# Optimization experiments

Hardware: AMD Instinct MI355X
Metric: run time of the kernel (lower is better)

## Reference

```python
import jax, jax.numpy as jnp
import numpy as np

TEMPERATURE = 0.1
GAMMA = 0.5
LOSS_WEIGHT = 1.0
MAX_BATCH_SIZE = 5000
POS_DIST_THRESH = 1.0
NEG_SAMPLE_RATIO = 2.0
EPS_NORM = 1e-8   # torch cosine_similarity norm clamp
EPS_POS = 1e-6


def setup_inputs() -> dict:
    key = jax.random.key(0)
    k1, k2 = jax.random.split(key)
    N, D = 15000, 64
    features = jax.random.normal(k1, (N, D), dtype=jnp.float32)
    # xyz coords in a 20-unit box -> ~8 positive neighbors per point at thresh 1.0
    coords = jax.random.uniform(k2, (N, 3), dtype=jnp.float32) * 20.0
    # all points are power-line class (label 2) so M = N statically
    labels = jnp.full((N,), 2, dtype=jnp.int32)
    return {"features": features, "labels": labels, "coords": coords}


def reference(features, labels, coords):
    # labels are all == 2 and none == ignore_index, so the boolean selections
    # (ignore_index filter, line_mask) are identities: line_feats = features.
    M = features.shape[0]
    # row-normalized features for cosine similarity (torch eps=1e-8 clamp)
    fnorm = features / jnp.maximum(
        jnp.linalg.norm(features, axis=1, keepdims=True), EPS_NORM)
    sq = jnp.sum(coords * coords, axis=1)  # [M]

    total_nce = jnp.float32(0.0)
    total_cont = jnp.float32(0.0)
    col = jnp.arange(M)[None, :]
    for start in range(0, M, MAX_BATCH_SIZE):
        end = min(start + MAX_BATCH_SIZE, M)
        B = end - start
        # [B, M] pairwise cosine similarity
        feat_sim = fnorm[start:end] @ fnorm.T
        # [B, M] euclidean cdist via ||a||^2 + ||b||^2 - 2 a.b
        d2 = sq[start:end, None] + sq[None, :] - 2.0 * (coords[start:end] @ coords.T)
        coord_dist = jnp.sqrt(jnp.maximum(d2, 0.0))
        pos = (coord_dist < POS_DIST_THRESH) & (coord_dist > 1e-6)
        posf = pos.astype(feat_sim.dtype)
        negf = 1.0 - posf

        exp_sim = jnp.exp(feat_sim / TEMPERATURE)
        # k = min(int(neg_sample_ratio * max positives per row), M); traced scalar
        max_neg = (NEG_SAMPLE_RATIO * pos.sum(axis=1).max()).astype(jnp.int32)
        k = jnp.minimum(max_neg, M)
        # top-k sum of masked negatives: full descending sort + length-k row mask
        vals = jnp.sort(exp_sim * negf, axis=1)[:, ::-1]
        sum_exp = jnp.sum(jnp.where(col < k, vals, 0.0), axis=1)

        pos_sum = jnp.sum(exp_sim * posf, axis=1)
        batch_nce = jnp.mean(-jnp.log(pos_sum / (sum_exp + pos_sum + EPS_POS)))
        batch_cont = jnp.mean(jnp.abs((1.0 - feat_sim) - coord_dist) * posf)

        total_nce = total_nce + batch_nce * B
        total_cont = total_cont + batch_cont * B

    loss = (total_nce / M + GAMMA * (total_cont / M)) * LOSS_WEIGHT
    return loss
```

## Files before the change

### kernel.cpp

```cpp
#include <hip/hip_runtime.h>
#include <math.h>

#define NPTS 15000
#define NPAD 15360
#define DIM 64
#define BATCH 5000
#define QT 64
#define NCH 4
#define NBLKQ 235
#define NGB (NBLKQ * NCH)
#define NPB 1875
#define BLKM 512
#define NT (NPAD / 16)
#define NTC (NT / NCH)
#define CAPE 12
#define NCELL 8000
#define NBIN 320
#define HW 160
#define GHW ((size_t)NBLKQ * QT * HW)
#define T_G 0.26f
#define KEY_BASE 0x3E80u

typedef __attribute__((ext_vector_type(8))) short bf16x8;
typedef __attribute__((ext_vector_type(4))) float f32x4;

__device__ __forceinline__ float bf2f(unsigned u) {
  return __uint_as_float(u << 16);
}

__global__ __launch_bounds__(256) void k_norm(const float* __restrict__ feat,
                                              const float* __restrict__ coords,
                                              unsigned short* __restrict__ fbf,
                                              float4* __restrict__ c4,
                                              uint4* __restrict__ ghist4,
                                              int* __restrict__ batch_max,
                                              float* __restrict__ out) {
  unsigned gz = blockIdx.x * 256 + threadIdx.x;
  if (gz < (unsigned)(GHW / 4)) ghist4[gz] = make_uint4(0, 0, 0, 0);
  if (gz == 0) { out[0] = 0.0f; batch_max[0] = 0; batch_max[1] = 0; batch_max[2] = 0; }
  int i = blockIdx.x * 4 + (threadIdx.x >> 6);
  int d = threadIdx.x & 63;
  float v = (i < NPTS) ? feat[i * DIM + d] : 0.0f;
  float ss = v * v;
#pragma unroll
  for (int off = 32; off; off >>= 1) ss += __shfl_down(ss, off);
  ss = __shfl(ss, 0);
  float m = fmaxf(sqrtf(ss), 1e-8f);
  float nv = v / m;
  unsigned u = __float_as_uint(nv);
  fbf[i * DIM + d] = (unsigned short)((u + 0x7FFFu + ((u >> 16) & 1u)) >> 16);
  if (d == 0) {
    float cx = (i < NPTS) ? coords[i * 3] : 0.0f;
    float cy = (i < NPTS) ? coords[i * 3 + 1] : 0.0f;
    float cz = (i < NPTS) ? coords[i * 3 + 2] : 0.0f;
    c4[i] = make_float4(cx, cy, cz, cx * cx + cy * cy + cz * cz);
  }
}

__device__ __forceinline__ int cell_of(float4 c) {
  int cx = min(19, max(0, (int)c.x));
  int cy = min(19, max(0, (int)c.y));
  int cz = min(19, max(0, (int)c.z));
  return cx + 20 * (cy + 20 * cz);
}

__global__ __launch_bounds__(1024) void k_cells(const float4* __restrict__ c4,
                                                int* __restrict__ cell_start,
                                                int* __restrict__ cell_cnt,
                                                int* __restrict__ pts) {
  __shared__ int s_cnt[NCELL];
  __shared__ int s_ptr[NCELL];
  __shared__ int sw[16];
  int tid = threadIdx.x, lane = tid & 63, wv = tid >> 6;
  for (int x = tid; x < NCELL; x += 1024) s_cnt[x] = 0;
  __syncthreads();
  for (int i = tid; i < NPTS; i += 1024) atomicAdd(&s_cnt[cell_of(c4[i])], 1);
  __syncthreads();
  int run = 0;
  for (int c = 0; c < NCELL; c += 1024) {
    int idx = c + tid;
    int v = (idx < NCELL) ? s_cnt[idx] : 0;
    int inc = v;
#pragma unroll
    for (int off = 1; off < 64; off <<= 1) {
      int o = __shfl_up(inc, off);
      if (lane >= off) inc += o;
    }
    if (lane == 63) sw[wv] = inc;
    __syncthreads();
    int woff = 0, tot = 0;
#pragma unroll
    for (int w = 0; w < 16; ++w) {
      int s = sw[w];
      if (w < wv) woff += s;
      tot += s;
    }
    __syncthreads();
    int excl = run + woff + inc - v;
    if (idx < NCELL) {
      cell_start[idx] = excl;
      cell_cnt[idx] = v;
      s_ptr[idx] = excl;
    }
    run += tot;
  }
  __syncthreads();
  for (int i = tid; i < NPTS; i += 1024) {
    int ix = atomicAdd(&s_ptr[cell_of(c4[i])], 1);
    pts[ix] = i;
  }
}

union SMem {
  unsigned hist[QT * HW];
  struct { int ec[8]; unsigned short ek[8][CAPE]; int pc[8]; } p;
};

__global__ __launch_bounds__(BLKM, 4) void k_main(const unsigned short* __restrict__ fbf,
                                                  const float4* __restrict__ c4,
                                                  const int* __restrict__ cell_start,
                                                  const int* __restrict__ cell_cnt,
                                                  const int* __restrict__ pts,
                                                  unsigned* __restrict__ ghist,
                                                  float* __restrict__ g_ps,
                                                  float* __restrict__ row_cont,
                                                  int* __restrict__ batch_max,
                                                  unsigned short* __restrict__ excl_keys,
                                                  int* __restrict__ excl_cnt) {
  __shared__ SMem sm;
  int bx = blockIdx.x;
  int tid = threadIdx.x;
  int wv = tid >> 6, lane = tid & 63;

  if (bx < NGB) {
    int tile = bx >> 2, ch = bx & 3;
    int i0 = tile * QT;
    int l15 = lane & 15, quad = lane >> 4;

    for (int x = tid; x < QT * HW; x += BLKM) sm.hist[x] = 0;

    bf16x8 aL[4], aH[4];
#pragma unroll
    for (int m = 0; m < 4; ++m) {
      const unsigned short* qrow = fbf + (size_t)(i0 + m * 16 + l15) * DIM + quad * 8;
      aL[m] = *(const bf16x8*)qrow;
      aH[m] = *(const bf16x8*)(qrow + 32);
    }
    __syncthreads();

    int tEnd = (ch + 1) * NTC;
    int t = ch * NTC + wv;
    const unsigned short* jr = fbf + (size_t)(t * 16 + l15) * DIM + quad * 8;
    bf16x8 bLo = *(const bf16x8*)jr;
    bf16x8 bHi = *(const bf16x8*)(jr + 32);
    for (; t < tEnd; t += 8) {
      int tn = (t + 8 < tEnd) ? t + 8 : t;
      const unsigned short* nr = fbf + (size_t)(tn * 16 + l15) * DIM + quad * 8;
      bf16x8 nLo = *(const bf16x8*)nr;
      bf16x8 nHi = *(const bf16x8*)(nr + 32);
      f32x4 acc[4];
#pragma unroll
      for (int m = 0; m < 4; ++m) {
        f32x4 a = {0.f, 0.f, 0.f, 0.f};
        a = __builtin_amdgcn_mfma_f32_16x16x32_bf16(aL[m], bLo, a, 0, 0, 0);
        a = __builtin_amdgcn_mfma_f32_16x16x32_bf16(aH[m], bHi, a, 0, 0, 0);
        acc[m] = a;
      }
#pragma unroll
      for (int m = 0; m < 4; ++m) {
#pragma unroll
        for (int r = 0; r < 4; ++r) {
          float s = acc[m][r];
          if (s >= T_G) {
            int q = m * 16 + quad * 4 + r;
            unsigned bin = (__float_as_uint(s) >> 16) - KEY_BASE;
            atomicAdd(&sm.hist[q * HW + (bin >> 1)], 1u << ((bin & 1) << 4));
          }
        }
      }
      bLo = nLo;
      bHi = nHi;
    }
    __syncthreads();

    unsigned* gh = ghist + (size_t)i0 * HW;
    for (int x = tid; x < QT * HW; x += BLKM) {
      unsigned v = sm.hist[x];
      if (v) atomicAdd(&gh[x], v);
    }
  } else {
    int bp = bx - NGB;
    int i = bp * 8 + wv;
    if (lane == 0) sm.p.ec[wv] = 0;
    float4 ci = c4[i];
    int cx = min(19, max(0, (int)ci.x));
    int cy = min(19, max(0, (int)ci.y));
    int cz = min(19, max(0, (int)ci.z));
    float psum = 0.f, csum = 0.f;
    int pc = 0;
    if (lane < 27) {
      int gx = cx + lane % 3 - 1, gy = cy + (lane / 3) % 3 - 1, gz = cz + lane / 9 - 1;
      if (gx >= 0 && gx < 20 && gy >= 0 && gy < 20 && gz >= 0 && gz < 20) {
        int cell = gx + 20 * (gy + 20 * gz);
        int s0 = cell_start[cell], e0 = s0 + cell_cnt[cell];
        for (int p = s0; p < e0; ++p) {
          int j = pts[p];
          if (j == i) continue;
          float4 cj = c4[j];
          float ddx = ci.x - cj.x, ddy = ci.y - cj.y, ddz = ci.z - cj.z;
          float d2 = ddx * ddx + ddy * ddy + ddz * ddz;
          if (d2 < 1.0f) {
            const unsigned short* fi = fbf + (size_t)i * DIM;
            const unsigned short* fj = fbf + (size_t)j * DIM;
            float dot = 0.f;
#pragma unroll
            for (int chv = 0; chv < 8; ++chv) {
              bf16x8 a = *(const bf16x8*)(fi + chv * 8);
              bf16x8 b = *(const bf16x8*)(fj + chv * 8);
#pragma unroll
              for (int e = 0; e < 8; ++e)
                dot = fmaf(bf2f((unsigned short)a[e] & 0xFFFFu),
                           bf2f((unsigned short)b[e] & 0xFFFFu), dot);
            }
            pc++;
            psum += expf(dot * 10.0f);
            csum += fabsf((1.0f - dot) - sqrtf(d2));
            if (dot >= T_G) {
              int ix = atomicAdd(&sm.p.ec[wv], 1);
              if (ix < CAPE) sm.p.ek[wv][ix] = (unsigned short)(__float_as_uint(dot) >> 16);
            }
          }
        }
      }
    }
#pragma unroll
    for (int off = 32; off; off >>= 1) {
      psum += __shfl_down(psum, off);
      csum += __shfl_down(csum, off);
      pc += __shfl_down(pc, off);
    }
    if (lane == 0) sm.p.pc[wv] = pc;
    __syncthreads();
    int ec = min(sm.p.ec[wv], CAPE);
    if (lane == 0) {
      g_ps[i] = psum;
      row_cont[i] = csum;
      excl_cnt[i] = ec;
    }
    for (int x = lane; x < ec; x += 64) excl_keys[(size_t)i * CAPE + x] = sm.p.ek[wv][x];
    if (tid == 0) {
      int m = 0;
#pragma unroll
      for (int w = 0; w < 8; ++w) m = max(m, sm.p.pc[w]);
      atomicMax(&batch_max[(bp * 8) / BATCH], m);
    }
  }
}

__global__ __launch_bounds__(BLKM) void k_select(const unsigned* __restrict__ ghist,
                                                 const float* __restrict__ g_ps,
                                                 const float* __restrict__ row_cont,
                                                 const int* __restrict__ batch_max,
                                                 const unsigned short* __restrict__ excl_keys,
                                                 const int* __restrict__ excl_cnt,
                                                 float* __restrict__ out) {
  int i0 = blockIdx.x * QT;
  int tid = threadIdx.x;
  int wv = tid >> 6, lane = tid & 63;
  float a_acc = 0.f, b_acc = 0.f;

  for (int qq = 0; qq < 8; ++qq) {
    int iq = i0 + wv * 8 + qq;
    if (iq >= NPTS) continue;
    int kq = min((int)(2.0f * (float)batch_max[iq / BATCH]), NPTS);
    int e = 5 * lane;
    const unsigned* hw_ = ghist + (size_t)iq * HW + (e >> 1);
    unsigned w0 = hw_[0], w1 = hw_[1], w2 = hw_[2];
    bool odd = (lane & 1) != 0;
    int h0 = (int)(odd ? (w0 >> 16) : (w0 & 0xFFFFu));
    int h1 = (int)(odd ? (w1 & 0xFFFFu) : (w0 >> 16));
    int h2 = (int)(odd ? (w1 >> 16) : (w1 & 0xFFFFu));
    int h3 = (int)(odd ? (w2 & 0xFFFFu) : (w1 >> 16));
    int h4 = (int)(odd ? (w2 >> 16) : (w2 & 0xFFFFu));
    int ec = min(excl_cnt[iq], CAPE);
    for (int ee = 0; ee < ec; ++ee) {
      unsigned key = excl_keys[(size_t)iq * CAPE + ee];
      unsigned bin = key - KEY_BASE;
      if (bin > NBIN - 1u) bin = NBIN - 1u;
      int c = (int)bin - e;
      if (c == 0) h0 = max(h0 - 1, 0);
      else if (c == 1) h1 = max(h1 - 1, 0);
      else if (c == 2) h2 = max(h2 - 1, 0);
      else if (c == 3) h3 = max(h3 - 1, 0);
      else if (c == 4) h4 = max(h4 - 1, 0);
    }
    int lsum = h0 + h1 + h2 + h3 + h4;
    int pre = lsum;
#pragma unroll
    for (int off = 1; off < 64; off <<= 1) {
      int o = __shfl_up(pre, off);
      if (lane >= off) pre += o;
    }
    int total = __shfl(pre, 63);
    int tke = min(kq, total);
    int cum = total - pre;
    float se = 0.0f;
    unsigned kb = KEY_BASE + (unsigned)e;
    {
      int tk4 = min(max(tke - cum, 0), h4); cum += h4;
      int tk3 = min(max(tke - cum, 0), h3); cum += h3;
      int tk2 = min(max(tke - cum, 0), h2); cum += h2;
      int tk1 = min(max(tke - cum, 0), h1); cum += h1;
      int tk0 = min(max(tke - cum, 0), h0);
      if (tk4) se += (float)tk4 * expf(10.0f * bf2f(kb + 4));
      if (tk3) se += (float)tk3 * expf(10.0f * bf2f(kb + 3));
      if (tk2) se += (float)tk2 * expf(10.0f * bf2f(kb + 2));
      if (tk1) se += (float)tk1 * expf(10.0f * bf2f(kb + 1));
      if (tk0) se += (float)tk0 * expf(10.0f * bf2f(kb + 0));
    }
#pragma unroll
    for (int off = 32; off; off >>= 1) se += __shfl_down(se, off);
    if (lane == 0) {
      float ps = g_ps[iq];
      float nce = -logf(ps / (se + ps + 1e-6f));
      if (!(nce < 1e30f)) nce = 0.0f;
      a_acc += nce;
      b_acc += row_cont[iq];
    }
  }
  __shared__ float sa[8], sb[8];
  if (lane == 0) { sa[wv] = a_acc; sb[wv] = b_acc; }
  __syncthreads();
  if (tid == 0) {
    float a = 0.f, b = 0.f;
#pragma unroll
    for (int w = 0; w < 8; ++w) { a += sa[w]; b += sb[w]; }
    atomicAdd(out, a / 15000.0f + 0.5f * ((b / 15000.0f) / 15000.0f));
  }
}

extern "C" void kernel_launch(void* const* d_in, const int* in_sizes, int n_in,
                              void* d_out, int out_size, void* d_ws, size_t ws_size,
                              hipStream_t stream) {
  const float* feat   = (const float*)d_in[0];
  const float* coords = (const float*)d_in[2];
  float* out = (float*)d_out;

  char* ws              = (char*)d_ws;
  unsigned short* fbf   = (unsigned short*)ws;
  float4* c4            = (float4*)(fbf + NPAD * DIM);
  float* row_cont       = (float*)(c4 + NPAD);
  float* g_ps           = row_cont + NPTS;
  int*   excl_ct        = (int*)(g_ps + NPTS);
  unsigned short* exclk = (unsigned short*)(excl_ct + NPTS);
  int*   batch_max      = (int*)(exclk + (size_t)NPTS * CAPE);
  unsigned* ghist       = (unsigned*)(batch_max + 4);
  int*   cell_start     = (int*)(ghist + GHW);
  int*   cell_cnt       = cell_start + NCELL;
  int*   pts            = cell_cnt + NCELL;

  k_norm<<<dim3(NPAD / 4), dim3(256), 0, stream>>>(feat, coords, fbf, c4,
                                                   (uint4*)ghist, batch_max, out);
  k_cells<<<dim3(1), dim3(1024), 0, stream>>>(c4, cell_start, cell_cnt, pts);
  k_main<<<dim3(NGB + NPB), dim3(BLKM), 0, stream>>>(fbf, c4, cell_start, cell_cnt, pts,
                                                     ghist, g_ps, row_cont, batch_max,
                                                     exclk, excl_ct);
  k_select<<<dim3(NBLKQ), dim3(BLKM), 0, stream>>>(ghist, g_ps, row_cont, batch_max,
                                                   exclk, excl_ct, out);
}
```

Baseline: 209.6 us.

## Compact positive pairs into shared list and compute dots one-per-lane in fp32

The positive-pair path now gathers neighbor indices and squared distances into a per-wave shared list, then lets each lane compute one pair's dot product. Before, at most 27 lanes each walked a cell serially, computing dots as they went. Dots now use the original fp32 features scaled by a precomputed inverse norm instead of bf16, which removes divergent serial work and conversion cost. The trade-offs are extra shared memory, a cap of 64 positives per row that silently drops extras, and a precision change in the positive sums.

```diff
diff --git a/kernel.cpp b/kernel.cpp
--- a/kernel.cpp
+++ b/kernel.cpp
@@ -14,6 +14,7 @@
 #define NT (NPAD / 16)
 #define NTC (NT / NCH)
 #define CAPE 12
+#define CAPP 64
 #define NCELL 8000
 #define NBIN 320
 #define HW 160
@@ -32,6 +33,7 @@
                                               const float* __restrict__ coords,
                                               unsigned short* __restrict__ fbf,
                                               float4* __restrict__ c4,
+                                              float* __restrict__ inv_m,
                                               uint4* __restrict__ ghist4,
                                               int* __restrict__ batch_max,
                                               float* __restrict__ out) {
@@ -54,6 +56,7 @@
     float cy = (i < NPTS) ? coords[i * 3 + 1] : 0.0f;
     float cz = (i < NPTS) ? coords[i * 3 + 2] : 0.0f;
     c4[i] = make_float4(cx, cy, cz, cx * cx + cy * cy + cz * cz);
+    if (i < NPTS) inv_m[i] = 1.0f / m;
   }
 }
 
@@ -113,10 +116,17 @@
 
 union SMem {
   unsigned hist[QT * HW];
-  struct { int ec[8]; unsigned short ek[8][CAPE]; int pc[8]; } p;
+  struct {
+    int np[8]; int ec[8]; int pc[8];
+    int list[8][CAPP];
+    float d2s[8][CAPP];
+    unsigned short ek[8][CAPE];
+  } p;
 };
 
 __global__ __launch_bounds__(BLKM, 4) void k_main(const unsigned short* __restrict__ fbf,
+                                                  const float* __restrict__ feat,
+                                                  const float* __restrict__ inv_m,
                                                   const float4* __restrict__ c4,
                                                   const int* __restrict__ cell_start,
                                                   const int* __restrict__ cell_cnt,
@@ -191,13 +201,11 @@
   } else {
     int bp = bx - NGB;
     int i = bp * 8 + wv;
-    if (lane == 0) sm.p.ec[wv] = 0;
+    if (lane == 0) { sm.p.np[wv] = 0; sm.p.ec[wv] = 0; }
     float4 ci = c4[i];
     int cx = min(19, max(0, (int)ci.x));
     int cy = min(19, max(0, (int)ci.y));
     int cz = min(19, max(0, (int)ci.z));
-    float psum = 0.f, csum = 0.f;
-    int pc = 0;
     if (lane < 27) {
       int gx = cx + lane % 3 - 1, gy = cy + (lane / 3) % 3 - 1, gz = cz + lane / 9 - 1;
       if (gx >= 0 && gx < 20 && gy >= 0 && gy < 20 && gz >= 0 && gz < 20) {
@@ -210,44 +218,49 @@
           float ddx = ci.x - cj.x, ddy = ci.y - cj.y, ddz = ci.z - cj.z;
           float d2 = ddx * ddx + ddy * ddy + ddz * ddz;
           if (d2 < 1.0f) {
-            const unsigned short* fi = fbf + (size_t)i * DIM;
-            const unsigned short* fj = fbf + (size_t)j * DIM;
-            float dot = 0.f;
-#pragma unroll
-            for (int chv = 0; chv < 8; ++chv) {
-              bf16x8 a = *(const bf16x8*)(fi + chv * 8);
-              bf16x8 b = *(const bf16x8*)(fj + chv * 8);
-#pragma unroll
-              for (int e = 0; e < 8; ++e)
-                dot = fmaf(bf2f((unsigned short)a[e] & 0xFFFFu),
-                           bf2f((unsigned short)b[e] & 0xFFFFu), dot);
-            }
-            pc++;
-            psum += expf(dot * 10.0f);
-            csum += fabsf((1.0f - dot) - sqrtf(d2));
-            if (dot >= T_G) {
-              int ix = atomicAdd(&sm.p.ec[wv], 1);
-              if (ix < CAPE) sm.p.ek[wv][ix] = (unsigned short)(__float_as_uint(dot) >> 16);
-            }
+            int slot = atomicAdd(&sm.p.np[wv], 1);
+            if (slot < CAPP) { sm.p.list[wv][slot] = j; sm.p.d2s[wv][slot] = d2; }
           }
         }
+      }
+    }
+    int npt = sm.p.np[wv];
+    int np = min(npt, CAPP);
+    float psum = 0.f, csum = 0.f;
+    if (lane < np) {
+      int j = sm.p.list[wv][lane];
+      float d2 = sm.p.d2s[wv][lane];
+      const float4* fi4 = (const float4*)(feat + (size_t)i * DIM);
+      const float4* fj4 = (const float4*)(feat + (size_t)j * DIM);
+      float dot = 0.f;
+#pragma unroll
+      for (int c = 0; c < 16; ++c) {
+        float4 a = fi4[c];
+        float4 b = fj4[c];
+        dot = fmaf(a.w, b.w, fmaf(a.z, b.z, fmaf(a.y, b.y, fmaf(a.x, b.x, dot))));
+      }
+      dot *= inv_m[i] * inv_m[j];
+      psum = expf(dot * 10.0f);
+      csum = fabsf((1.0f - dot) - sqrtf(d2));
+      if (dot >= T_G) {
+        int ix = atomicAdd(&sm.p.ec[wv], 1);
+        if (ix < CAPE) sm.p.ek[wv][ix] = (unsigned short)(__float_as_uint(dot) >> 16);
       }
     }
 #pragma unroll
     for (int off = 32; off; off >>= 1) {
       psum += __shfl_down(psum, off);
       csum += __shfl_down(csum, off);
-      pc += __shfl_down(pc, off);
-    }
-    if (lane == 0) sm.p.pc[wv] = pc;
-    __syncthreads();
+    }
     int ec = min(sm.p.ec[wv], CAPE);
     if (lane == 0) {
       g_ps[i] = psum;
       row_cont[i] = csum;
       excl_cnt[i] = ec;
+      sm.p.pc[wv] = npt;
     }
     for (int x = lane; x < ec; x += 64) excl_keys[(size_t)i * CAPE + x] = sm.p.ek[wv][x];
+    __syncthreads();
     if (tid == 0) {
       int m = 0;
 #pragma unroll
@@ -354,15 +367,17 @@
   int*   excl_ct        = (int*)(g_ps + NPTS);
   unsigned short* exclk = (unsigned short*)(excl_ct + NPTS);
   int*   batch_max      = (int*)(exclk + (size_t)NPTS * CAPE);
-  unsigned* ghist       = (unsigned*)(batch_max + 4);
+  float* inv_m          = (float*)(batch_max + 4);
+  unsigned* ghist       = (unsigned*)(inv_m + NPTS);
   int*   cell_start     = (int*)(ghist + GHW);
   int*   cell_cnt       = cell_start + NCELL;
   int*   pts            = cell_cnt + NCELL;
 
-  k_norm<<<dim3(NPAD / 4), dim3(256), 0, stream>>>(feat, coords, fbf, c4,
+  k_norm<<<dim3(NPAD / 4), dim3(256), 0, stream>>>(feat, coords, fbf, c4, inv_m,
                                                    (uint4*)ghist, batch_max, out);
   k_cells<<<dim3(1), dim3(1024), 0, stream>>>(c4, cell_start, cell_cnt, pts);
-  k_main<<<dim3(NGB + NPB), dim3(BLKM), 0, stream>>>(fbf, c4, cell_start, cell_cnt, pts,
+  k_main<<<dim3(NGB + NPB), dim3(BLKM), 0, stream>>>(fbf, feat, inv_m, c4,
+                                                     cell_start, cell_cnt, pts,
                                                      ghist, g_ps, row_cont, batch_max,
                                                      exclk, excl_ct);
   k_select<<<dim3(NBLKQ), dim3(BLKM), 0, stream>>>(ghist, g_ps, row_cont, batch_max,
```

Measured after the change: 192.1 us. 1.09x faster.
